# Optimization experiments

Hardware: AMD Instinct MI355X
Metric: run time of the kernel (lower is better)

Reference implementation:

```python
import jax, jax.numpy as jnp
import numpy as np

ALPHA = 0.9
BETA = 0.1
GAMMA = 0.1
EPS = 1e-8  # torch cosine_similarity eps


def setup_inputs() -> dict:
    key = jax.random.key(0)
    k1, k2 = jax.random.split(key)
    N = 8192
    y = jax.random.normal(k1, (N, 1), dtype=jnp.float32)
    labels = jax.random.normal(k2, (N, 1), dtype=jnp.float32)
    return {"y": y, "labels": labels}


def reference(y, labels):
    # --- MSE ---
    mse_loss = jnp.mean((y - labels) ** 2)

    # --- cosine similarity along dim=1 (torch semantics: each norm clamped by eps) ---
    yn = jnp.linalg.norm(y, axis=1)        # [N]
    ln = jnp.linalg.norm(labels, axis=1)   # [N]
    cos = jnp.sum(y * labels, axis=1) / (jnp.maximum(yn, EPS) * jnp.maximum(ln, EPS))
    similarity_loss = 1.0 - jnp.mean(cos)

    # --- vectorized pairwise margin ranking over i<j ---
    ys = y[:, 0]       # [N]
    ls = labels[:, 0]  # [N]
    dy = ys[:, None] - ys[None, :]   # [N, N]
    dl = ls[:, None] - ls[None, :]   # [N, N]
    # r_ij = 1 if labels[i] > labels[j], -1 if <, else sign(y[i]-y[j])
    r = jnp.where(dl > 0, 1.0, jnp.where(dl < 0, -1.0, jnp.sign(dy)))
    N = ys.shape[0]
    upper = jnp.triu(jnp.ones((N, N), dtype=bool), k=1)  # i<j pairs
    hinge = jnp.maximum(0.0, -r * dy)
    margin_ranking_loss = jnp.sum(jnp.where(upper, hinge, 0.0)) / (N * (N - 1) / 2)

    return ALPHA * mse_loss + BETA * margin_ranking_loss + GAMMA * similarity_loss
```

## Files before the change

### kernel.cpp

```cpp
#include <hip/hip_runtime.h>
#include <hip/hip_bf16.h>


constexpr int BLOCK = 256;
constexpr int M_PER = 4;
constexpr int ITILE = BLOCK * M_PER;
constexpr int JCH   = 64;

#define EPS_F 1e-8f

__global__ __launch_bounds__(BLOCK) void combined_loss_pair_kernel(
    const float* __restrict__ y, const float* __restrict__ l, int N, int JT,
    float* __restrict__ hpart,
    float* __restrict__ mpart,
    float* __restrict__ cpart)
{
    __shared__ float sy[JCH];
    __shared__ float sl[JCH];
    __shared__ float red[BLOCK / 64];

    const int bx  = blockIdx.x;
    const int it  = bx / JT;
    const int jt  = bx % JT;
    const int tid = threadIdx.x;

    float yi[M_PER], li[M_PER];
    bool  vm[M_PER];
#pragma unroll
    for (int m = 0; m < M_PER; ++m) {
        const int i = it * ITILE + m * BLOCK + tid;
        vm[m] = (i < N);
        yi[m] = vm[m] ? y[i] : 0.f;
        li[m] = vm[m] ? l[i] : 0.f;
    }

    const int j0   = jt * JCH;
    const int jcnt = min(JCH, N - j0);
    if (tid < JCH) {
        const bool vj = (tid < jcnt);
        sy[tid] = vj ? y[j0 + tid] : 0.f;
        sl[tid] = vj ? l[j0 + tid] : 0.f;
    }
    __syncthreads();

    float A[M_PER], B[M_PER];
#pragma unroll
    for (int m = 0; m < M_PER; ++m) { A[m] = 0.f; B[m] = 0.f; }

#define PROC(yj, lj)                                         \
    {                                                        \
        _Pragma("unroll")                                    \
        for (int m = 0; m < M_PER; ++m) {                    \
            const float u = yi[m] - (yj);                    \
            A[m] += fabsf(u);                                \
            B[m] += (li[m] < (lj)) ? u : -u;                 \
        }                                                    \
    }

    const int kv = jcnt & ~3;
#pragma unroll 4
    for (int k = 0; k < kv; k += 4) {
        const float4 y4 = *reinterpret_cast<const float4*>(&sy[k]);
        const float4 l4 = *reinterpret_cast<const float4*>(&sl[k]);
        PROC(y4.x, l4.x);
        PROC(y4.y, l4.y);
        PROC(y4.z, l4.z);
        PROC(y4.w, l4.w);
    }
    for (int k = kv; k < jcnt; ++k) PROC(sy[k], sl[k]);
#undef PROC

    float h = 0.f;
#pragma unroll
    for (int m = 0; m < M_PER; ++m)
        if (vm[m]) h += 0.5f * (A[m] + B[m]);

    for (int o = 32; o > 0; o >>= 1) h += __shfl_down(h, o, 64);
    const int lane = tid & 63, wid = tid >> 6;
    if (lane == 0) red[wid] = h;
    __syncthreads();
    if (tid == 0) {
        float s = 0.f;
        for (int w = 0; w < BLOCK / 64; ++w) s += red[w];
        hpart[bx] = s;
    }
    __syncthreads();

    if (jt == 0) {
        float msum = 0.f, csum = 0.f;
#pragma unroll
        for (int m = 0; m < M_PER; ++m) {
            if (vm[m]) {
                const float d = yi[m] - li[m];
                msum += d * d;
                csum += (yi[m] * li[m]) /
                        (fmaxf(fabsf(yi[m]), EPS_F) * fmaxf(fabsf(li[m]), EPS_F));
            }
        }
        for (int o = 32; o > 0; o >>= 1) {
            msum += __shfl_down(msum, o, 64);
            csum += __shfl_down(csum, o, 64);
        }
        if (lane == 0) red[wid] = msum;
        __syncthreads();
        float mtot = 0.f;
        if (tid == 0) for (int w = 0; w < BLOCK / 64; ++w) mtot += red[w];
        __syncthreads();
        if (lane == 0) red[wid] = csum;
        __syncthreads();
        if (tid == 0) {
            float ctot = 0.f;
            for (int w = 0; w < BLOCK / 64; ++w) ctot += red[w];
            mpart[it] = mtot;
            cpart[it] = ctot;
        }
    }
}

__global__ __launch_bounds__(256) void combined_loss_finalize_kernel(
    const float* __restrict__ hpart, const float* __restrict__ mpart,
    const float* __restrict__ cpart, int nh, int nm, int N,
    float* __restrict__ out)
{
    double h = 0.0, m = 0.0, c = 0.0;
    for (int k = threadIdx.x; k < nh; k += blockDim.x) h += (double)hpart[k];
    for (int k = threadIdx.x; k < nm; k += blockDim.x) {
        m += (double)mpart[k];
        c += (double)cpart[k];
    }
    for (int o = 32; o > 0; o >>= 1) {
        h += __shfl_down(h, o, 64);
        m += __shfl_down(m, o, 64);
        c += __shfl_down(c, o, 64);
    }
    __shared__ double sh[4][3];
    const int lane = threadIdx.x & 63, wid = threadIdx.x >> 6;
    if (lane == 0) { sh[wid][0] = h; sh[wid][1] = m; sh[wid][2] = c; }
    __syncthreads();
    if (threadIdx.x == 0) {
        double H = 0, M = 0, C = 0;
        for (int w = 0; w < 4; ++w) { H += sh[w][0]; M += sh[w][1]; C += sh[w][2]; }
        const double Nd     = (double)N;
        const double mse    = M / Nd;
        const double pairs  = Nd * (Nd - 1.0) * 0.5;
        const double margin = (H * 0.5) / pairs;
        const double sim    = 1.0 - C / Nd;
        out[0] = (float)(0.9 * mse + 0.1 * margin + 0.1 * sim);
    }
}

extern "C" void kernel_launch(void* const* d_in, const int* in_sizes, int n_in,
                              void* d_out, int out_size, void* d_ws, size_t ws_size,
                              hipStream_t stream) {
    const float* y = (const float*)d_in[0];
    const float* l = (const float*)d_in[1];
    const int N = in_sizes[0];

    const int IT = (N + ITILE - 1) / ITILE;
    const int JT = (N + JCH - 1) / JCH;

    float* hpart = (float*)d_ws;
    float* mpart = hpart + (size_t)IT * JT;
    float* cpart = mpart + IT;

    combined_loss_pair_kernel<<<IT * JT, BLOCK, 0, stream>>>(y, l, N, JT,
                                                             hpart, mpart, cpart);
    combined_loss_finalize_kernel<<<1, 256, 0, stream>>>(hpart, mpart, cpart,
                                                         IT * JT, IT, N,
                                                         (float*)d_out);
}
```

Measured before the change: 68.50 us.

## Fuse finalize into pair kernel via atomics and last-block reduction, double rows per thread

```diff
diff --git a/kernel.cpp b/kernel.cpp
--- a/kernel.cpp
+++ b/kernel.cpp
@@ -3,17 +3,18 @@
 
 
 constexpr int BLOCK = 256;
-constexpr int M_PER = 4;
+constexpr int M_PER = 8;
 constexpr int ITILE = BLOCK * M_PER;
 constexpr int JCH   = 64;
 
 #define EPS_F 1e-8f
 
-__global__ __launch_bounds__(BLOCK) void combined_loss_pair_kernel(
+__global__ __launch_bounds__(BLOCK) void combined_loss_fused_kernel(
     const float* __restrict__ y, const float* __restrict__ l, int N, int JT,
-    float* __restrict__ hpart,
-    float* __restrict__ mpart,
-    float* __restrict__ cpart)
+    int total_blocks,
+    float* __restrict__ acc,
+    unsigned int* __restrict__ done,
+    float* __restrict__ out)
 {
     __shared__ float sy[JCH];
     __shared__ float sl[JCH];
@@ -58,7 +59,6 @@
     }
 
     const int kv = jcnt & ~3;
-#pragma unroll 4
     for (int k = 0; k < kv; k += 4) {
         const float4 y4 = *reinterpret_cast<const float4*>(&sy[k]);
         const float4 l4 = *reinterpret_cast<const float4*>(&sl[k]);
@@ -79,13 +79,10 @@
     const int lane = tid & 63, wid = tid >> 6;
     if (lane == 0) red[wid] = h;
     __syncthreads();
-    if (tid == 0) {
-        float s = 0.f;
-        for (int w = 0; w < BLOCK / 64; ++w) s += red[w];
-        hpart[bx] = s;
-    }
-    __syncthreads();
+    float hblk = 0.f;
+    if (tid == 0) for (int w = 0; w < BLOCK / 64; ++w) hblk += red[w];
 
+    float mblk = 0.f, cblk = 0.f;
     if (jt == 0) {
         float msum = 0.f, csum = 0.f;
 #pragma unroll
@@ -101,51 +98,35 @@
             msum += __shfl_down(msum, o, 64);
             csum += __shfl_down(csum, o, 64);
         }
+        __syncthreads();
         if (lane == 0) red[wid] = msum;
         __syncthreads();
-        float mtot = 0.f;
-        if (tid == 0) for (int w = 0; w < BLOCK / 64; ++w) mtot += red[w];
+        if (tid == 0) for (int w = 0; w < BLOCK / 64; ++w) mblk += red[w];
         __syncthreads();
         if (lane == 0) red[wid] = csum;
         __syncthreads();
-        if (tid == 0) {
-            float ctot = 0.f;
-            for (int w = 0; w < BLOCK / 64; ++w) ctot += red[w];
-            mpart[it] = mtot;
-            cpart[it] = ctot;
+        if (tid == 0) for (int w = 0; w < BLOCK / 64; ++w) cblk += red[w];
+    }
+
+    if (tid == 0) {
+        atomicAdd(&acc[0], hblk);
+        if (jt == 0) {
+            atomicAdd(&acc[1], mblk);
+            atomicAdd(&acc[2], cblk);
         }
-    }
-}
-
-__global__ __launch_bounds__(256) void combined_loss_finalize_kernel(
-    const float* __restrict__ hpart, const float* __restrict__ mpart,
-    const float* __restrict__ cpart, int nh, int nm, int N,
-    float* __restrict__ out)
-{
-    double h = 0.0, m = 0.0, c = 0.0;
-    for (int k = threadIdx.x; k < nh; k += blockDim.x) h += (double)hpart[k];
-    for (int k = threadIdx.x; k < nm; k += blockDim.x) {
-        m += (double)mpart[k];
-        c += (double)cpart[k];
-    }
-    for (int o = 32; o > 0; o >>= 1) {
-        h += __shfl_down(h, o, 64);
-        m += __shfl_down(m, o, 64);
-        c += __shfl_down(c, o, 64);
-    }
-    __shared__ double sh[4][3];
-    const int lane = threadIdx.x & 63, wid = threadIdx.x >> 6;
-    if (lane == 0) { sh[wid][0] = h; sh[wid][1] = m; sh[wid][2] = c; }
-    __syncthreads();
-    if (threadIdx.x == 0) {
-        double H = 0, M = 0, C = 0;
-        for (int w = 0; w < 4; ++w) { H += sh[w][0]; M += sh[w][1]; C += sh[w][2]; }
-        const double Nd     = (double)N;
-        const double mse    = M / Nd;
-        const double pairs  = Nd * (Nd - 1.0) * 0.5;
-        const double margin = (H * 0.5) / pairs;
-        const double sim    = 1.0 - C / Nd;
-        out[0] = (float)(0.9 * mse + 0.1 * margin + 0.1 * sim);
+        __threadfence();
+        const unsigned int old = atomicAdd(done, 1u);
+        if (old == (unsigned int)(total_blocks - 1)) {
+            const double H = (double)atomicAdd(&acc[0], 0.f);
+            const double M = (double)atomicAdd(&acc[1], 0.f);
+            const double C = (double)atomicAdd(&acc[2], 0.f);
+            const double Nd     = (double)N;
+            const double mse    = M / Nd;
+            const double pairs  = Nd * (Nd - 1.0) * 0.5;
+            const double margin = (H * 0.5) / pairs;
+            const double sim    = 1.0 - C / Nd;
+            out[0] = (float)(0.9 * mse + 0.1 * margin + 0.1 * sim);
+        }
     }
 }
 
@@ -158,14 +139,12 @@
 
     const int IT = (N + ITILE - 1) / ITILE;
     const int JT = (N + JCH - 1) / JCH;
+    const int total_blocks = IT * JT;
 
-    float* hpart = (float*)d_ws;
-    float* mpart = hpart + (size_t)IT * JT;
-    float* cpart = mpart + IT;
+    float* acc         = (float*)d_ws;
+    unsigned int* done = (unsigned int*)(acc + 3);
 
-    combined_loss_pair_kernel<<<IT * JT, BLOCK, 0, stream>>>(y, l, N, JT,
-                                                             hpart, mpart, cpart);
-    combined_loss_finalize_kernel<<<1, 256, 0, stream>>>(hpart, mpart, cpart,
-                                                         IT * JT, IT, N,
-                                                         (float*)d_out);
+    hipMemsetAsync(d_ws, 0, 4 * sizeof(float), stream);
+    combined_loss_fused_kernel<<<total_blocks, BLOCK, 0, stream>>>(
+        y, l, N, JT, total_blocks, acc, done, (float*)d_out);
 }
```

Result: slower. 76.39 us (+11.5%).
